# Kernel optimization log

Hardware: AMD Instinct MI355X
Metric: run time of the kernel (lower is better)

Reference implementation:

```python
import jax, jax.numpy as jnp
import numpy as np

DIM = 1024
N_HEADS = 16
HEAD_DIM = DIM // N_HEADS


def setup_inputs() -> dict:
    key = jax.random.key(0)
    ks = jax.random.split(key, 5)
    B, L = 2, 2048
    q = jax.random.normal(ks[0], (B, L, DIM), dtype=jnp.float32)
    # nn.Linear weights: shape [out_features, in_features], applied as x @ W.T
    scale = 1.0 / np.sqrt(DIM)
    Wq = jax.random.normal(ks[1], (DIM, DIM), dtype=jnp.float32) * scale
    Wk = jax.random.normal(ks[2], (DIM, DIM), dtype=jnp.float32) * scale
    Wv = jax.random.normal(ks[3], (DIM, DIM), dtype=jnp.float32) * scale
    Wo = jax.random.normal(ks[4], (DIM, DIM), dtype=jnp.float32) * scale
    return {"q": q, "Wq": Wq, "Wk": Wk, "Wv": Wv, "Wo": Wo}


def reference(q, Wq, Wk, Wv, Wo):
    B, L, _ = q.shape
    kv = q  # self-attention (kv=None path)
    # projections: x @ W.T, then split heads: b l (h d) -> b h l d
    def split_heads(x):
        return x.reshape(B, L, N_HEADS, HEAD_DIM).transpose(0, 2, 1, 3)
    qh = split_heads(q @ Wq.T)
    kh = split_heads(kv @ Wk.T)
    vh = split_heads(kv @ Wv.T)
    # scaled dot-product attention; scale = sqrt(head_dim)
    scores = jnp.einsum('bhid,bhjd->bhij', qh, kh) / jnp.sqrt(
        jnp.asarray(HEAD_DIM, dtype=qh.dtype))
    attn = jax.nn.softmax(scores, axis=-1)
    out = jnp.einsum('bhij,bhjd->bhid', attn, vh)
    # b h l d -> b l (h d)
    out = out.transpose(0, 2, 1, 3).reshape(B, L, DIM)
    return out @ Wo.T
```

## Files before the change

### kernel.cpp

```cpp
#include <hip/hip_runtime.h>


#define DIMN 1024
#define NH 16
#define HD 64
#define BB 2
#define LL 2048

typedef float f32x4 __attribute__((ext_vector_type(4)));
typedef short s16x8 __attribute__((ext_vector_type(8)));

#define QSCALE 0.18033688011112042f

static __device__ __forceinline__ unsigned short f2bf(float f) {
  unsigned u = __float_as_uint(f);
  u += 0x7fffu + ((u >> 16) & 1u);
  return (unsigned short)(u >> 16);
}
static __device__ __forceinline__ unsigned packbf2(float lo, float hi) {
  return (unsigned)f2bf(lo) | ((unsigned)f2bf(hi) << 16);
}
static __device__ __forceinline__ float xexp2(float x) {
#if __has_builtin(__builtin_amdgcn_exp2f)
  return __builtin_amdgcn_exp2f(x);
#else
  return exp2f(x);
#endif
}
static __device__ __forceinline__ s16x8 cvt8(float4 a, float4 b) {
  s16x8 r;
  r[0] = (short)f2bf(a.x); r[1] = (short)f2bf(a.y);
  r[2] = (short)f2bf(a.z); r[3] = (short)f2bf(a.w);
  r[4] = (short)f2bf(b.x); r[5] = (short)f2bf(b.y);
  r[6] = (short)f2bf(b.z); r[7] = (short)f2bf(b.w);
  return r;
}
static __device__ __forceinline__ void gld16(const unsigned short* g,
                                             unsigned short* l) {
#if __has_builtin(__builtin_amdgcn_global_load_lds)
  __builtin_amdgcn_global_load_lds(
      (const __attribute__((address_space(1))) void*)g,
      (__attribute__((address_space(3))) void*)l, 16, 0, 0);
#else
  ((uint4*)l)[threadIdx.x & 63] = ((const uint4*)g)[0];
#endif
}

static __device__ __forceinline__ int vpos(int s128) {
  return (s128 & 0x60) | ((s128 & 0x0C) << 1) | ((s128 & 0x10) >> 2) | (s128 & 3);
}

__global__ __launch_bounds__(256) void cvt_all(
    const float* __restrict__ X, const float* __restrict__ Wq,
    const float* __restrict__ Wk, const float* __restrict__ Wv,
    const float* __restrict__ Wo, unsigned short* __restrict__ out) {
  const int blk = blockIdx.x;
  const float* src;
  unsigned short* dst;
  size_t off;
  if (blk < 2048) {
    src = X; dst = out; off = (size_t)blk * 2048;
  } else {
    int s = (blk - 2048) >> 9;
    src = (s == 0) ? Wq : (s == 1) ? Wk : (s == 2) ? Wv : Wo;
    dst = out + ((size_t)1 << 22) + (size_t)s * (1u << 20);
    off = (size_t)((blk - 2048) & 511) * 2048;
  }
  size_t i = off + (size_t)threadIdx.x * 8;
  float4 v0 = *(const float4*)(src + i);
  float4 v1 = *(const float4*)(src + i + 4);
  uint4 o;
  o.x = packbf2(v0.x, v0.y); o.y = packbf2(v0.z, v0.w);
  o.z = packbf2(v1.x, v1.y); o.w = packbf2(v1.z, v1.w);
  *(uint4*)(dst + i) = o;
}

__global__ __launch_bounds__(256) void gemm_qkv(
    const unsigned short* __restrict__ Xb, const unsigned short* __restrict__ Wb,
    unsigned short* __restrict__ Qb, unsigned short* __restrict__ Kb,
    unsigned short* __restrict__ VT) {
  __shared__ __align__(16) unsigned short Al[128 * 64];
  __shared__ __align__(16) unsigned short Bl[128 * 64];
  const int lin = blockIdx.x;
  const int xcd = lin & 7, sblk = lin >> 3;
  const int m0 = ((xcd & 3) * 8 + (sblk & 7)) * 128;
  const int n0g = ((xcd >> 2) * 12 + (sblk >> 3)) * 128;
  const int sel = n0g >> 10;
  const int tid = threadIdx.x;
  const int w = tid >> 6, lane = tid & 63;
  const int c = lane & 15, quad = lane >> 4;
  const int wm = (w & 1) * 64, wn = (w >> 1) * 64;

  f32x4 zero = {0.f, 0.f, 0.f, 0.f};
  f32x4 acc[4][4];
#pragma unroll
  for (int i = 0; i < 4; ++i)
#pragma unroll
    for (int j = 0; j < 4; ++j) acc[i][j] = zero;

  const int l8 = lane >> 3, p8 = lane & 7;
  const unsigned short* gA = Xb + (size_t)(m0 + w * 8 + l8) * DIMN + ((p8 ^ l8) * 8);
  const unsigned short* gB = Wb + (size_t)(n0g + w * 8 + l8) * DIMN + ((p8 ^ l8) * 8);
  unsigned short* lA = Al + (w * 8) * 64;
  unsigned short* lB = Bl + (w * 8) * 64;
  const int c7 = c & 7;

  for (int k0 = 0; k0 < DIMN; k0 += 64) {
    __syncthreads();
#pragma unroll
    for (int r = 0; r < 4; ++r) {
      gld16(gA + k0 + (size_t)(r * 32) * DIMN, lA + r * 32 * 64);
      gld16(gB + k0 + (size_t)(r * 32) * DIMN, lB + r * 32 * 64);
    }
    __syncthreads();
#pragma unroll
    for (int f = 0; f < 2; ++f) {
      const int rd = ((f * 4 + quad) ^ c7) * 8;
      s16x8 a[4], b[4];
#pragma unroll
      for (int i = 0; i < 4; ++i)
        a[i] = *(const s16x8*)&Al[(wm + i * 16 + c) * 64 + rd];
#pragma unroll
      for (int j = 0; j < 4; ++j)
        b[j] = *(const s16x8*)&Bl[(wn + j * 16 + c) * 64 + rd];
      if (sel != 2) {
#pragma unroll
        for (int i = 0; i < 4; ++i)
#pragma unroll
          for (int j = 0; j < 4; ++j)
            acc[i][j] = __builtin_amdgcn_mfma_f32_16x16x32_bf16(b[j], a[i], acc[i][j], 0, 0, 0);
      } else {
#pragma unroll
        for (int i = 0; i < 4; ++i)
#pragma unroll
          for (int j = 0; j < 4; ++j)
            acc[i][j] = __builtin_amdgcn_mfma_f32_16x16x32_bf16(a[i], b[j], acc[i][j], 0, 0, 0);
      }
    }
  }

  const int n0 = n0g & 1023;
  if (sel != 2) {
    unsigned short* Out = (sel == 0) ? Qb : Kb;
    const float scale = (sel == 0) ? QSCALE : 1.0f;
    const int bi = (m0 + wm) >> 11;
#pragma unroll
    for (int i = 0; i < 4; ++i) {
      const int li = (m0 + wm + i * 16 + c) & 2047;
#pragma unroll
      for (int j = 0; j < 4; ++j) {
        const int nq = n0 + wn + j * 16 + quad * 4;
        const int h = nq >> 6, d = nq & 63;
        uint2 st;
        st.x = packbf2(acc[i][j][0] * scale, acc[i][j][1] * scale);
        st.y = packbf2(acc[i][j][2] * scale, acc[i][j][3] * scale);
        *(uint2*)&Out[(((size_t)bi * NH + h) * LL + li) * HD + d] = st;
      }
    }
  } else {
    const int bi = m0 >> 11;
    const int mlo = m0 & 2047;
#pragma unroll
    for (int i = 0; i < 4; ++i) {
      const int pos = mlo + vpos(wm + i * 16 + quad * 4);
#pragma unroll
      for (int j = 0; j < 4; ++j) {
        const int nv = n0 + wn + j * 16 + c;
        const int h = nv >> 6, d = nv & 63;
        uint2 st;
        st.x = packbf2(acc[i][j][0], acc[i][j][1]);
        st.y = packbf2(acc[i][j][2], acc[i][j][3]);
        *(uint2*)&VT[(((size_t)bi * NH + h) * HD + d) * LL + pos] = st;
      }
    }
  }
}

__global__ __launch_bounds__(256) void gemm_o(
    const unsigned short* __restrict__ A, const unsigned short* __restrict__ Wob,
    float* __restrict__ Out) {
  __shared__ __align__(16) unsigned short Al[128 * 64];
  __shared__ __align__(16) unsigned short Bl[64 * 64];
  const int lin = blockIdx.x;
  const int xcd = lin & 7, sblk = lin >> 3;
  const int m0 = ((sblk >> 4) * 8 + xcd) * 128;
  const int n0 = (sblk & 15) * 64;
  const int tid = threadIdx.x;
  const int w = tid >> 6, lane = tid & 63;
  const int c = lane & 15, quad = lane >> 4;
  const int wm = (w & 1) * 64, wn = (w >> 1) * 32;

  f32x4 zero = {0.f, 0.f, 0.f, 0.f};
  f32x4 acc[4][2];
#pragma unroll
  for (int i = 0; i < 4; ++i)
#pragma unroll
    for (int j = 0; j < 2; ++j) acc[i][j] = zero;

  const int l8 = lane >> 3, p8 = lane & 7;
  const unsigned short* gA = A + (size_t)(m0 + w * 8 + l8) * DIMN + ((p8 ^ l8) * 8);
  const unsigned short* gB = Wob + (size_t)(n0 + w * 8 + l8) * DIMN + ((p8 ^ l8) * 8);
  unsigned short* lA = Al + (w * 8) * 64;
  unsigned short* lB = Bl + (w * 8) * 64;
  const int c7 = c & 7;

  for (int k0 = 0; k0 < DIMN; k0 += 64) {
    __syncthreads();
#pragma unroll
    for (int r = 0; r < 4; ++r)
      gld16(gA + k0 + (size_t)(r * 32) * DIMN, lA + r * 32 * 64);
#pragma unroll
    for (int r = 0; r < 2; ++r)
      gld16(gB + k0 + (size_t)(r * 32) * DIMN, lB + r * 32 * 64);
    __syncthreads();
#pragma unroll
    for (int f = 0; f < 2; ++f) {
      const int rd = ((f * 4 + quad) ^ c7) * 8;
      s16x8 a[4], b[2];
#pragma unroll
      for (int i = 0; i < 4; ++i)
        a[i] = *(const s16x8*)&Al[(wm + i * 16 + c) * 64 + rd];
#pragma unroll
      for (int j = 0; j < 2; ++j)
        b[j] = *(const s16x8*)&Bl[(wn + j * 16 + c) * 64 + rd];
#pragma unroll
      for (int i = 0; i < 4; ++i)
#pragma unroll
        for (int j = 0; j < 2; ++j)
          acc[i][j] = __builtin_amdgcn_mfma_f32_16x16x32_bf16(a[i], b[j], acc[i][j], 0, 0, 0);
    }
  }

#pragma unroll
  for (int i = 0; i < 4; ++i)
#pragma unroll
    for (int j = 0; j < 2; ++j)
#pragma unroll
      for (int r = 0; r < 4; ++r)
        Out[(size_t)(m0 + wm + i * 16 + quad * 4 + r) * DIMN + n0 + wn + j * 16 + c] =
            acc[i][j][r];
}

__global__ __launch_bounds__(512) void attn10(
    const unsigned short* __restrict__ Qb, const unsigned short* __restrict__ Kb,
    const unsigned short* __restrict__ VT, unsigned short* __restrict__ AO) {
  __shared__ __align__(16) unsigned short Kl[2][2][64 * 64];
  __shared__ __align__(16) unsigned short Vtl[2][2][64 * 64];

  const int lin = blockIdx.x;
  const int xcd = lin & 7, sblk = lin >> 3;
  const int bh = (sblk >> 3) * 8 + xcd;
  const int qblk = sblk & 7;
  const int tid = threadIdx.x;
  const int w = tid >> 6, lane = tid & 63;
  const int half = w >> 2, wl = w & 3;
  const int c = lane & 15, quad = lane >> 4;
  const int q0 = qblk * 256 + wl * 16;

  const unsigned short* Qh = Qb + (size_t)bh * LL * HD;
  const unsigned short* Kh = Kb + (size_t)bh * LL * HD + (size_t)half * 1024 * HD;
  const unsigned short* Vh = VT + (size_t)bh * HD * LL + half * 1024;

  s16x8 qf[4][2];
#pragma unroll
  for (int s = 0; s < 4; ++s) {
    qf[s][0] = *(const s16x8*)(Qh + (size_t)(q0 + s * 64 + c) * HD + quad * 8);
    qf[s][1] = *(const s16x8*)(Qh + (size_t)(q0 + s * 64 + c) * HD + 32 + quad * 8);
  }

  f32x4 zero = {0.f, 0.f, 0.f, 0.f};
  f32x4 o[4][4];
  float lsum[4] = {0.f, 0.f, 0.f, 0.f};
#pragma unroll
  for (int s = 0; s < 4; ++s)
#pragma unroll
    for (int dc = 0; dc < 4; ++dc) o[s][dc] = zero;

  const int l8 = lane >> 3, p8 = lane & 7;
  const unsigned short* gK = Kh + (size_t)(wl * 16 + l8) * HD + ((p8 ^ l8) * 8);
  const int vr = wl * 16 + l8;
  const unsigned short* gV = Vh + (size_t)vr * LL + ((p8 ^ l8) * 8);

  const int c7 = c & 7;
  const int kpa = (quad ^ c7) * 8;
  const int kpb = ((quad + 4) ^ c7) * 8;

#define STAGE(buf, kv)                                                        \
  do {                                                                        \
    unsigned short* lK_ = &Kl[half][buf][(wl * 16) * 64];                     \
    unsigned short* lV_ = &Vtl[half][buf][(wl * 16) * 64];                    \
    gld16(gK + (size_t)(kv) * HD, lK_);                                       \
    gld16(gK + (size_t)((kv) + 8) * HD, lK_ + 8 * 64);                        \
    gld16(gV + (kv), lV_);                                                    \
    gld16(gV + (size_t)8 * LL + (kv), lV_ + 8 * 64);                          \
  } while (0)

  STAGE(0, 0);

  for (int it = 0; it < 16; ++it) {
    __syncthreads();
    if (it + 1 < 16) STAGE((it + 1) & 1, (it + 1) * 64);
    const unsigned short* Kt = &Kl[half][it & 1][0];
    const unsigned short* Vt = &Vtl[half][it & 1][0];

    s16x8 kf[4][2];
#pragma unroll
    for (int t4 = 0; t4 < 4; ++t4) {
      const unsigned short* kr = Kt + (t4 * 16 + c) * 64;
      kf[t4][0] = *(const s16x8*)(kr + kpa);
      kf[t4][1] = *(const s16x8*)(kr + kpb);
    }

    s16x8 pf[4][2];
#pragma unroll
    for (int s = 0; s < 4; ++s) {
      f32x4 sc[4];
#pragma unroll
      for (int t4 = 0; t4 < 4; ++t4) {
        sc[t4] = __builtin_amdgcn_mfma_f32_16x16x32_bf16(kf[t4][0], qf[s][0], zero, 0, 0, 0);
        sc[t4] = __builtin_amdgcn_mfma_f32_16x16x32_bf16(kf[t4][1], qf[s][1], sc[t4], 0, 0, 0);
      }
      float p[4][4];
      float a0 = 0.f, a1 = 0.f;
#pragma unroll
      for (int t4 = 0; t4 < 4; ++t4)
#pragma unroll
        for (int r = 0; r < 4; ++r) {
          float e = xexp2(sc[t4][r]);
          p[t4][r] = e;
          if (t4 & 1) a1 += e; else a0 += e;
        }
      lsum[s] += a0 + a1;
#pragma unroll
      for (int kh = 0; kh < 2; ++kh) {
        unsigned pu[4];
        pu[0] = __builtin_amdgcn_perm(__float_as_uint(p[2 * kh][1]),
                                      __float_as_uint(p[2 * kh][0]), 0x07060302u);
        pu[1] = __builtin_amdgcn_perm(__float_as_uint(p[2 * kh][3]),
                                      __float_as_uint(p[2 * kh][2]), 0x07060302u);
        pu[2] = __builtin_amdgcn_perm(__float_as_uint(p[2 * kh + 1][1]),
                                      __float_as_uint(p[2 * kh + 1][0]), 0x07060302u);
        pu[3] = __builtin_amdgcn_perm(__float_as_uint(p[2 * kh + 1][3]),
                                      __float_as_uint(p[2 * kh + 1][2]), 0x07060302u);
        pf[s][kh] = *(const s16x8*)pu;
      }
    }

#pragma unroll
    for (int kh = 0; kh < 2; ++kh) {
#pragma unroll
      for (int dc = 0; dc < 4; ++dc) {
        s16x8 vf = *(const s16x8*)(Vt + (dc * 16 + c) * 64 +
                                   (((kh * 4 + quad) ^ c7) * 8));
#pragma unroll
        for (int s = 0; s < 4; ++s)
          o[s][dc] = __builtin_amdgcn_mfma_f32_16x16x32_bf16(vf, pf[s][kh], o[s][dc], 0, 0, 0);
      }
    }
  }
#undef STAGE

#pragma unroll
  for (int s = 0; s < 4; ++s) {
    lsum[s] += __shfl_xor(lsum[s], 16);
    lsum[s] += __shfl_xor(lsum[s], 32);
  }

  f32x4* ob4 = (f32x4*)&Kl[0][0][0];
  float* lb = (float*)&Vtl[0][0][0];
  const int bi = bh >> 4, h = bh & 15;

#pragma unroll
  for (int pass = 0; pass < 2; ++pass) {
    __syncthreads();
    if (half == 1) {
#pragma unroll
      for (int sp = 0; sp < 2; ++sp) {
        const int s = pass * 2 + sp;
#pragma unroll
        for (int dc = 0; dc < 4; ++dc)
          ob4[((wl * 2 + sp) * 4 + dc) * 64 + lane] = o[s][dc];
        lb[(wl * 2 + sp) * 64 + lane] = lsum[s];
      }
    }
    __syncthreads();
    if (half == 0) {
#pragma unroll
      for (int sp = 0; sp < 2; ++sp) {
        const int s = pass * 2 + sp;
        const float l = lsum[s] + lb[(wl * 2 + sp) * 64 + lane];
        const float inv = 1.0f / l;
        unsigned short* dst =
            AO + ((size_t)bi * LL + q0 + s * 64 + c) * DIMN + h * HD + quad * 4;
#pragma unroll
        for (int dc = 0; dc < 4; ++dc) {
          f32x4 sum = o[s][dc] + ob4[((wl * 2 + sp) * 4 + dc) * 64 + lane];
          uint2 st;
          st.x = packbf2(sum[0] * inv, sum[1] * inv);
          st.y = packbf2(sum[2] * inv, sum[3] * inv);
          *(uint2*)(dst + dc * 16) = st;
        }
      }
    }
  }
}

__global__ __launch_bounds__(64) void qkv_proj_f(
    const float* __restrict__ X, const float* __restrict__ Wq,
    const float* __restrict__ Wk, const float* __restrict__ Wv,
    unsigned short* __restrict__ Qb, unsigned short* __restrict__ Kb,
    unsigned short* __restrict__ VT) {
  const int m0 = blockIdx.x * 64;
  const int n0g = blockIdx.y * 64;
  const int sel = n0g >> 10;
  const int n0 = n0g & 1023;
  const float* W = (sel == 0) ? Wq : (sel == 1) ? Wk : Wv;
  const int lane = threadIdx.x;
  const int c = lane & 15, quad = lane >> 4;

  f32x4 zero = {0.f, 0.f, 0.f, 0.f};
  f32x4 acc[4][4];
#pragma unroll
  for (int i = 0; i < 4; ++i)
#pragma unroll
    for (int j = 0; j < 4; ++j) acc[i][j] = zero;

  const float* ab = X + (size_t)(m0 + c) * DIMN + quad * 8;
  const float* bb = W + (size_t)(n0 + c) * DIMN + quad * 8;

  for (int k0 = 0; k0 < DIMN; k0 += 32) {
    s16x8 a[4], b[4];
#pragma unroll
    for (int i = 0; i < 4; ++i) {
      const float* pp = ab + i * 16 * DIMN + k0;
      a[i] = cvt8(*(const float4*)pp, *(const float4*)(pp + 4));
    }
#pragma unroll
    for (int j = 0; j < 4; ++j) {
      const float* pp = bb + j * 16 * DIMN + k0;
      b[j] = cvt8(*(const float4*)pp, *(const float4*)(pp + 4));
    }
    if (sel != 2) {
#pragma unroll
      for (int i = 0; i < 4; ++i)
#pragma unroll
        for (int j = 0; j < 4; ++j)
          acc[i][j] = __builtin_amdgcn_mfma_f32_16x16x32_bf16(a[i], b[j], acc[i][j], 0, 0, 0);
    } else {
#pragma unroll
      for (int i = 0; i < 4; ++i)
#pragma unroll
        for (int j = 0; j < 4; ++j)
          acc[i][j] = __builtin_amdgcn_mfma_f32_16x16x32_bf16(b[j], a[i], acc[i][j], 0, 0, 0);
    }
  }

  if (sel != 2) {
    unsigned short* Out = (sel == 0) ? Qb : Kb;
    const float scale = (sel == 0) ? QSCALE : 1.0f;
#pragma unroll
    for (int i = 0; i < 4; ++i)
#pragma unroll
      for (int j = 0; j < 4; ++j)
#pragma unroll
        for (int r = 0; r < 4; ++r) {
          int row = m0 + i * 16 + quad * 4 + r;
          int nl = n0 + j * 16 + c;
          int bi = row >> 11, li = row & 2047;
          int h = nl >> 6, d = nl & 63;
          Out[(((size_t)bi * NH + h) * LL + li) * HD + d] = f2bf(acc[i][j][r] * scale);
        }
  } else {
#pragma unroll
    for (int i = 0; i < 4; ++i) {
#pragma unroll
      for (int j = 0; j < 4; ++j)
#pragma unroll
        for (int r = 0; r < 4; ++r) {
          int n = n0 + j * 16 + quad * 4 + r;
          int s128 = (m0 & 64) + i * 16 + c;
          int m = (m0 & ~127) + vpos(s128);
          int h = n >> 6, d = n & 63;
          int bi = m0 >> 11;
          VT[(((size_t)bi * NH + h) * HD + d) * LL + (m & 2047)] = f2bf(acc[i][j][r]);
        }
    }
  }
}

__global__ __launch_bounds__(64) void o_proj_f(
    const unsigned short* __restrict__ A, const float* __restrict__ Wo,
    float* __restrict__ Out) {
  const int m0 = blockIdx.x * 64, n0 = blockIdx.y * 64;
  const int lane = threadIdx.x;
  const int c = lane & 15, quad = lane >> 4;

  f32x4 zero = {0.f, 0.f, 0.f, 0.f};
  f32x4 acc[4][4];
#pragma unroll
  for (int i = 0; i < 4; ++i)
#pragma unroll
    for (int j = 0; j < 4; ++j) acc[i][j] = zero;

  const unsigned short* ab = A + (size_t)(m0 + c) * DIMN + quad * 8;
  const float* bb = Wo + (size_t)(n0 + c) * DIMN + quad * 8;

  for (int k0 = 0; k0 < DIMN; k0 += 32) {
    s16x8 a[4], b[4];
#pragma unroll
    for (int i = 0; i < 4; ++i) a[i] = *(const s16x8*)(ab + i * 16 * DIMN + k0);
#pragma unroll
    for (int j = 0; j < 4; ++j) {
      const float* pp = bb + j * 16 * DIMN + k0;
      b[j] = cvt8(*(const float4*)pp, *(const float4*)(pp + 4));
    }
#pragma unroll
    for (int i = 0; i < 4; ++i)
#pragma unroll
      for (int j = 0; j < 4; ++j)
        acc[i][j] = __builtin_amdgcn_mfma_f32_16x16x32_bf16(a[i], b[j], acc[i][j], 0, 0, 0);
  }

#pragma unroll
  for (int i = 0; i < 4; ++i)
#pragma unroll
    for (int j = 0; j < 4; ++j)
#pragma unroll
      for (int r = 0; r < 4; ++r)
        Out[(size_t)(m0 + i * 16 + quad * 4 + r) * DIMN + n0 + j * 16 + c] = acc[i][j][r];
}

extern "C" void kernel_launch(void* const* d_in, const int* in_sizes, int n_in,
                              void* d_out, int out_size, void* d_ws, size_t ws_size,
                              hipStream_t stream) {
  const float* X = (const float*)d_in[0];
  const float* Wq = (const float*)d_in[1];
  const float* Wk = (const float*)d_in[2];
  const float* Wv = (const float*)d_in[3];
  const float* Wo = (const float*)d_in[4];
  float* Out = (float*)d_out;

  const size_t M1 = (size_t)1 << 20;
  unsigned short* ws16 = (unsigned short*)d_ws;

  if (ws_size >= (size_t)48 * 1024 * 1024) {
    unsigned short* Xb = ws16;
    unsigned short* Wb = ws16 + 4 * M1;
    unsigned short* Qb = ws16 + 8 * M1;
    unsigned short* Kb = ws16 + 12 * M1;
    unsigned short* VT = ws16 + 16 * M1;
    unsigned short* AO = ws16 + 20 * M1;
    cvt_all<<<4096, 256, 0, stream>>>(X, Wq, Wk, Wv, Wo, ws16);
    gemm_qkv<<<768, 256, 0, stream>>>(Xb, Wb, Qb, Kb, VT);
    attn10<<<256, 512, 0, stream>>>(Qb, Kb, VT, AO);
    gemm_o<<<512, 256, 0, stream>>>(AO, Wb + 3 * M1, Out);
  } else {
    unsigned short* Qb = ws16;
    unsigned short* Kb = ws16 + 4 * M1;
    unsigned short* VT = ws16 + 8 * M1;
    unsigned short* AO = ws16 + 12 * M1;
    qkv_proj_f<<<dim3(64, 48), 64, 0, stream>>>(X, Wq, Wk, Wv, Qb, Kb, VT);
    attn10<<<256, 512, 0, stream>>>(Qb, Kb, VT, AO);
    o_proj_f<<<dim3(64, 16), 64, 0, stream>>>(AO, Wo, Out);
  }
}
```

Baseline: 175.3 us.

## Split attention into 512 blocks of 256 threads with 128-query tiles

Reworks the attention kernel so each block has 4 waves (2 per KV half) covering 128 queries, instead of 8 waves covering 256 queries, and doubles the grid to 512 blocks. Each wave now stages four K and four V rows per tile, and the cross-half reduction finishes in a single pass. The aim is a finer work split across the CUs with less per-block synchronisation. In exchange, each K/V tile loaded into LDS is reused by fewer queries.

```diff
diff --git a/kernel.cpp b/kernel.cpp
--- a/kernel.cpp
+++ b/kernel.cpp
@@ -241,7 +241,7 @@
             acc[i][j][r];
 }
 
-__global__ __launch_bounds__(512) void attn10(
+__global__ __launch_bounds__(256) void attn11(
     const unsigned short* __restrict__ Qb, const unsigned short* __restrict__ Kb,
     const unsigned short* __restrict__ VT, unsigned short* __restrict__ AO) {
   __shared__ __align__(16) unsigned short Kl[2][2][64 * 64];
@@ -249,13 +249,13 @@
 
   const int lin = blockIdx.x;
   const int xcd = lin & 7, sblk = lin >> 3;
-  const int bh = (sblk >> 3) * 8 + xcd;
-  const int qblk = sblk & 7;
+  const int bh = (sblk >> 4) * 8 + xcd;
+  const int qi = sblk & 15;
   const int tid = threadIdx.x;
   const int w = tid >> 6, lane = tid & 63;
-  const int half = w >> 2, wl = w & 3;
+  const int half = w >> 1, wl2 = w & 1;
   const int c = lane & 15, quad = lane >> 4;
-  const int q0 = qblk * 256 + wl * 16;
+  const int qbase = qi * 128 + wl2 * 16;
 
   const unsigned short* Qh = Qb + (size_t)bh * LL * HD;
   const unsigned short* Kh = Kb + (size_t)bh * LL * HD + (size_t)half * 1024 * HD;
@@ -264,8 +264,8 @@
   s16x8 qf[4][2];
 #pragma unroll
   for (int s = 0; s < 4; ++s) {
-    qf[s][0] = *(const s16x8*)(Qh + (size_t)(q0 + s * 64 + c) * HD + quad * 8);
-    qf[s][1] = *(const s16x8*)(Qh + (size_t)(q0 + s * 64 + c) * HD + 32 + quad * 8);
+    qf[s][0] = *(const s16x8*)(Qh + (size_t)(qbase + s * 32 + c) * HD + quad * 8);
+    qf[s][1] = *(const s16x8*)(Qh + (size_t)(qbase + s * 32 + c) * HD + 32 + quad * 8);
   }
 
   f32x4 zero = {0.f, 0.f, 0.f, 0.f};
@@ -277,9 +277,8 @@
     for (int dc = 0; dc < 4; ++dc) o[s][dc] = zero;
 
   const int l8 = lane >> 3, p8 = lane & 7;
-  const unsigned short* gK = Kh + (size_t)(wl * 16 + l8) * HD + ((p8 ^ l8) * 8);
-  const int vr = wl * 16 + l8;
-  const unsigned short* gV = Vh + (size_t)vr * LL + ((p8 ^ l8) * 8);
+  const unsigned short* gK = Kh + (size_t)(wl2 * 32 + l8) * HD + ((p8 ^ l8) * 8);
+  const unsigned short* gV = Vh + (size_t)(wl2 * 32 + l8) * LL + ((p8 ^ l8) * 8);
 
   const int c7 = c & 7;
   const int kpa = (quad ^ c7) * 8;
@@ -287,12 +286,14 @@
 
 #define STAGE(buf, kv)                                                        \
   do {                                                                        \
-    unsigned short* lK_ = &Kl[half][buf][(wl * 16) * 64];                     \
-    unsigned short* lV_ = &Vtl[half][buf][(wl * 16) * 64];                    \
-    gld16(gK + (size_t)(kv) * HD, lK_);                                       \
-    gld16(gK + (size_t)((kv) + 8) * HD, lK_ + 8 * 64);                        \
-    gld16(gV + (kv), lV_);                                                    \
-    gld16(gV + (size_t)8 * LL + (kv), lV_ + 8 * 64);                          \
+    unsigned short* lK_ = &Kl[half][buf][(wl2 * 32) * 64];                    \
+    unsigned short* lV_ = &Vtl[half][buf][(wl2 * 32) * 64];                   \
+    _Pragma("unroll")                                                         \
+    for (int r = 0; r < 4; ++r)                                               \
+      gld16(gK + (size_t)((kv) + r * 8) * HD, lK_ + r * 8 * 64);              \
+    _Pragma("unroll")                                                         \
+    for (int r = 0; r < 4; ++r)                                               \
+      gld16(gV + (size_t)(r * 8) * LL + (kv), lV_ + r * 8 * 64);              \
   } while (0)
 
   STAGE(0, 0);
@@ -370,36 +371,33 @@
   float* lb = (float*)&Vtl[0][0][0];
   const int bi = bh >> 4, h = bh & 15;
 
-#pragma unroll
-  for (int pass = 0; pass < 2; ++pass) {
-    __syncthreads();
-    if (half == 1) {
-#pragma unroll
-      for (int sp = 0; sp < 2; ++sp) {
-        const int s = pass * 2 + sp;
-#pragma unroll
-        for (int dc = 0; dc < 4; ++dc)
-          ob4[((wl * 2 + sp) * 4 + dc) * 64 + lane] = o[s][dc];
-        lb[(wl * 2 + sp) * 64 + lane] = lsum[s];
-      }
-    }
-    __syncthreads();
-    if (half == 0) {
-#pragma unroll
-      for (int sp = 0; sp < 2; ++sp) {
-        const int s = pass * 2 + sp;
-        const float l = lsum[s] + lb[(wl * 2 + sp) * 64 + lane];
-        const float inv = 1.0f / l;
-        unsigned short* dst =
-            AO + ((size_t)bi * LL + q0 + s * 64 + c) * DIMN + h * HD + quad * 4;
-#pragma unroll
-        for (int dc = 0; dc < 4; ++dc) {
-          f32x4 sum = o[s][dc] + ob4[((wl * 2 + sp) * 4 + dc) * 64 + lane];
-          uint2 st;
-          st.x = packbf2(sum[0] * inv, sum[1] * inv);
-          st.y = packbf2(sum[2] * inv, sum[3] * inv);
-          *(uint2*)(dst + dc * 16) = st;
-        }
+  __syncthreads();
+  if (half == 1) {
+#pragma unroll
+    for (int s = 0; s < 4; ++s) {
+      const int slot = wl2 * 4 + s;
+#pragma unroll
+      for (int dc = 0; dc < 4; ++dc)
+        ob4[(slot * 4 + dc) * 64 + lane] = o[s][dc];
+      lb[slot * 64 + lane] = lsum[s];
+    }
+  }
+  __syncthreads();
+  if (half == 0) {
+#pragma unroll
+    for (int s = 0; s < 4; ++s) {
+      const int slot = wl2 * 4 + s;
+      const float l = lsum[s] + lb[slot * 64 + lane];
+      const float inv = 1.0f / l;
+      unsigned short* dst =
+          AO + ((size_t)bi * LL + qbase + s * 32 + c) * DIMN + h * HD + quad * 4;
+#pragma unroll
+      for (int dc = 0; dc < 4; ++dc) {
+        f32x4 sum = o[s][dc] + ob4[(slot * 4 + dc) * 64 + lane];
+        uint2 st;
+        st.x = packbf2(sum[0] * inv, sum[1] * inv);
+        st.y = packbf2(sum[2] * inv, sum[3] * inv);
+        *(uint2*)(dst + dc * 16) = st;
       }
     }
   }
@@ -552,7 +550,7 @@
     unsigned short* AO = ws16 + 20 * M1;
     cvt_all<<<4096, 256, 0, stream>>>(X, Wq, Wk, Wv, Wo, ws16);
     gemm_qkv<<<768, 256, 0, stream>>>(Xb, Wb, Qb, Kb, VT);
-    attn10<<<256, 512, 0, stream>>>(Qb, Kb, VT, AO);
+    attn11<<<512, 256, 0, stream>>>(Qb, Kb, VT, AO);
     gemm_o<<<512, 256, 0, stream>>>(AO, Wb + 3 * M1, Out);
   } else {
     unsigned short* Qb = ws16;
@@ -560,7 +558,7 @@
     unsigned short* VT = ws16 + 8 * M1;
     unsigned short* AO = ws16 + 12 * M1;
     qkv_proj_f<<<dim3(64, 48), 64, 0, stream>>>(X, Wq, Wk, Wv, Qb, Kb, VT);
-    attn10<<<256, 512, 0, stream>>>(Qb, Kb, VT, AO);
+    attn11<<<512, 256, 0, stream>>>(Qb, Kb, VT, AO);
     o_proj_f<<<dim3(64, 16), 64, 0, stream>>>(AO, Wo, Out);
   }
 }
```

New measurement: 201.0 us. 14.6% more time.
